# Kernel tuning notes

Measured on AMD Instinct MI355X. Metric: run time of the kernel, lower is better.

Reference implementation:

```python
import jax, jax.numpy as jnp
import numpy as np

B, D, K, NCLS, BANK = 1024, 256, 8, 71, 32


def setup_inputs() -> dict:
    key = jax.random.key(0)
    ks = jax.random.split(key, 8)
    p = lambda k: jax.random.normal(k, (D, D), jnp.float32) * 0.02  # trunc_normal std=0.02 approx
    z = jnp.zeros((D,), jnp.float32)
    return {
        "target_token": jax.random.normal(ks[0], (B, D), jnp.float32),
        "fea_bank": jax.random.normal(ks[1], (NCLS, BANK, D), jnp.float32),
        "W_e1": p(ks[2]), "b_e1": z,
        "W_o1": p(ks[3]), "b_o1": z,
        "W_e2": p(ks[4]), "b_e2": z,
        "W_o2": p(ks[5]), "b_o2": z,
        "W_f1": p(ks[6]),
        "W_f2": p(ks[7]),
    }


def reference(target_token, fea_bank, W_e1, b_e1, W_o1, b_o1,
              W_e2, b_e2, W_o2, b_o2, W_f1, W_f2):
    lin = lambda x, W, b: x @ W.T + b  # torch nn.Linear convention

    # class-mean bank and euclidean cdist [B, NCLS]
    fea_mean = fea_bank.mean(axis=1)                              # [C, D]
    d2 = (jnp.sum(target_token ** 2, -1, keepdims=True)
          - 2.0 * target_token @ fea_mean.T
          + jnp.sum(fea_mean ** 2, -1))
    dist = jnp.sqrt(jnp.maximum(d2, 0.0))
    _, idx = jax.lax.top_k(-dist, K)                              # k smallest -> [B, K]

    # stage 1: blend with nearest class means
    nearest_means = fea_mean[idx]                                 # [B, K, D]
    e1 = jax.nn.gelu(lin(nearest_means - target_token[:, None], W_e1, b_e1),
                     approximate=False)
    w1 = e1 @ W_f1.T
    e1 = e1 * jax.nn.softmax(w1, axis=1)                          # softmax over K
    off1 = jnp.tanh(lin(target_token[:, None] + e1, W_o1, b_o1))
    s1 = (1.0 + off1) * target_token[:, None]                     # [B, K, D]

    # stage 2: blend with full intra-class banks of selected classes
    feats = fea_bank[idx]                                         # [B, K, BANK, D]
    e2 = jax.nn.gelu(lin(feats - s1[:, :, None], W_e2, b_e2), approximate=False)
    w2 = e2 @ W_f2.T
    e2 = e2 * jax.nn.softmax(w2, axis=2)                          # softmax over BANK
    off2 = jnp.tanh(lin(s1[:, :, None] + e2, W_o2, b_o2))
    s2 = ((1.0 + off2) * s1[:, :, None]).sum(axis=2)              # [B, K, D]

    return (s1, s2)
```

## Files before the change

### kernel.cpp

```cpp
#include <hip/hip_runtime.h>
#include <hip/hip_bf16.h>

#define BB 1024
#define DD 256
#define KK 8
#define NCLS_ 71
#define BANK_ 32
#define BKROWS (BB*KK)
#define NBROWS (NCLS_*BANK_)

typedef __bf16 bf16x8 __attribute__((ext_vector_type(8)));
typedef __bf16 bf16x4 __attribute__((ext_vector_type(4)));
typedef float f32x4 __attribute__((ext_vector_type(4)));

__device__ __forceinline__ float gelu_fast(float x) {
    float z = __expf(-1.702f * x);
    return x * __builtin_amdgcn_rcpf(1.0f + z);
}
__device__ __forceinline__ float tanh_fast(float y) {
    float z = __expf(2.0f * y);
    return 1.0f - 2.0f * __builtin_amdgcn_rcpf(z + 1.0f);
}
__device__ __forceinline__ int swz(int row, int colByte) {
    return (row * 512 + colByte) ^ ((row & 7) << 4);
}

template<int MT, int NT>
__device__ __forceinline__ void gemm_tile(const __bf16* __restrict__ Wg,
                                          const char* Ab, int m_base, int n_base,
                                          int lane, f32x4 (&acc)[MT][NT])
{
    #pragma unroll
    for (int ks = 0; ks < 8; ++ks) {
        bf16x8 a[MT];
        #pragma unroll
        for (int mt = 0; mt < MT; ++mt) {
            int row = m_base + mt*16 + (lane & 15);
            int cb  = ks*64 + ((lane >> 4) << 4);
            a[mt] = *reinterpret_cast<const bf16x8*>(Ab + swz(row, cb));
        }
        #pragma unroll
        for (int nt = 0; nt < NT; ++nt) {
            int n  = n_base + nt*16 + (lane & 15);
            int k0 = ks*32 + ((lane >> 4) << 3);
            bf16x8 b = *reinterpret_cast<const bf16x8*>(Wg + n*DD + k0);
            #pragma unroll
            for (int mt = 0; mt < MT; ++mt)
                acc[mt][nt] = __builtin_amdgcn_mfma_f32_16x16x32_bf16(a[mt], b, acc[mt][nt], 0, 0, 0);
        }
    }
}

__global__ __launch_bounds__(256) void k_prep(
    const float* __restrict__ We1f, const float* __restrict__ Wo1f,
    const float* __restrict__ We2f, const float* __restrict__ Wo2f,
    const float* __restrict__ Wf1f, const float* __restrict__ Wf2f,
    const float* __restrict__ fb,
    __bf16* __restrict__ We1, __bf16* __restrict__ Wo1,
    __bf16* __restrict__ We2, __bf16* __restrict__ Wo2,
    __bf16* __restrict__ Wf1, __bf16* __restrict__ Wf2,
    __bf16* __restrict__ fbb, float* __restrict__ fmean)
{
    int b = blockIdx.x, tid = threadIdx.x;
    if (b < 384) {
        int w = b >> 6;
        const float* s; __bf16* d;
        switch (w) {
            case 0: s = We1f; d = We1; break;
            case 1: s = Wo1f; d = Wo1; break;
            case 2: s = We2f; d = We2; break;
            case 3: s = Wo2f; d = Wo2; break;
            case 4: s = Wf1f; d = Wf1; break;
            default: s = Wf2f; d = Wf2; break;
        }
        int i = (b & 63)*256 + tid;
        float4 v = reinterpret_cast<const float4*>(s)[i];
        bf16x4 o = {(__bf16)v.x, (__bf16)v.y, (__bf16)v.z, (__bf16)v.w};
        *reinterpret_cast<bf16x4*>(d + i*4) = o;
    } else if (b < 952) {
        int i = (b - 384)*256 + tid;
        float4 v = reinterpret_cast<const float4*>(fb)[i];
        bf16x4 o = {(__bf16)v.x, (__bf16)v.y, (__bf16)v.z, (__bf16)v.w};
        *reinterpret_cast<bf16x4*>(fbb + i*4) = o;
    } else {
        int c = b - 952, d = tid;
        float s = 0.f;
        #pragma unroll
        for (int j = 0; j < BANK_; ++j) s += fb[(c*BANK_ + j)*DD + d];
        fmean[c*DD + d] = s * (1.0f / BANK_);
    }
}

__global__ __launch_bounds__(128) void k_stage1(
    const float* __restrict__ tgt, const float* __restrict__ fmean,
    int* __restrict__ idxg,
    const __bf16* __restrict__ We1, const float* __restrict__ be1,
    const __bf16* __restrict__ Wf1,
    const __bf16* __restrict__ Wo1, const float* __restrict__ bo1,
    float* __restrict__ out_s1, __bf16* __restrict__ s1b)
{
    __shared__ __bf16 As[16*256];
    __shared__ float tl[256];
    __shared__ float d2s[NCLS_ + 1];
    __shared__ int cls[8];
    char* Ab = (char*)As;
    int tid = threadIdx.x, lane = tid & 63, wid = tid >> 6;
    int b = blockIdx.x;
    if (tid < 64) reinterpret_cast<float4*>(tl)[tid] = reinterpret_cast<const float4*>(tgt + b*DD)[tid];
    {
        uint4 zz = {0u,0u,0u,0u};
        #pragma unroll
        for (int i = 0; i < 2; ++i) {
            int f = i*128 + tid;
            int row = 8 + (f >> 5), c = f & 31;
            *reinterpret_cast<uint4*>(Ab + swz(row, c*16)) = zz;
        }
    }
    __syncthreads();
    {
        float t0 = tl[lane], t1 = tl[64+lane], t2 = tl[128+lane], t3 = tl[192+lane];
        int cbeg = wid*36, cend = cbeg + 36 - wid;
        for (int c = cbeg; c < cend; ++c) {
            const float* m = fmean + c*DD;
            float a0 = t0 - m[lane], a1 = t1 - m[64+lane];
            float a2 = t2 - m[128+lane], a3 = t3 - m[192+lane];
            float p = a0*a0 + a1*a1 + a2*a2 + a3*a3;
            #pragma unroll
            for (int o = 32; o > 0; o >>= 1) p += __shfl_xor(p, o);
            if (lane == 0) d2s[c] = p;
        }
    }
    __syncthreads();
    if (tid == 0) {
        #pragma unroll
        for (int t = 0; t < KK; ++t) {
            float best = 3.4e38f; int bi = 0;
            for (int c = 0; c < NCLS_; ++c) { float v = d2s[c]; if (v < best) { best = v; bi = c; } }
            d2s[bi] = 3.4e38f;
            cls[t] = bi;
            idxg[b*KK + t] = bi;
        }
    }
    __syncthreads();
    int c16 = tid & 31, q = tid >> 5;
    #pragma unroll
    for (int i = 0; i < 2; ++i) {
        int row = i*4 + q;
        const float* mb = fmean + cls[row]*DD + c16*8;
        const float* tb = tl + c16*8;
        float4 m0 = *(const float4*)mb, m1 = *(const float4*)(mb+4);
        float4 t0 = *(const float4*)tb, t1 = *(const float4*)(tb+4);
        bf16x8 o = {(__bf16)(m0.x-t0.x), (__bf16)(m0.y-t0.y), (__bf16)(m0.z-t0.z), (__bf16)(m0.w-t0.w),
                    (__bf16)(m1.x-t1.x), (__bf16)(m1.y-t1.y), (__bf16)(m1.z-t1.z), (__bf16)(m1.w-t1.w)};
        *reinterpret_cast<bf16x8*>(Ab + swz(row, c16*16)) = o;
    }
    __syncthreads();
    int n_base = wid * 128;
    int qr = lane >> 4;
    const f32x4 z = {0.f, 0.f, 0.f, 0.f};
    f32x4 acc[1][8];
    #pragma unroll
    for (int nt = 0; nt < 8; ++nt) acc[0][nt] = z;
    gemm_tile<1,8>(We1, Ab, 0, n_base, lane, acc);
    float e1reg[8][4];
    #pragma unroll
    for (int nt = 0; nt < 8; ++nt)
        #pragma unroll
        for (int r = 0; r < 4; ++r) {
            int col = n_base + nt*16 + (lane & 15);
            e1reg[nt][r] = gelu_fast(acc[0][nt][r] + be1[col]);
        }
    __syncthreads();
    if (qr < 2)
        #pragma unroll
        for (int nt = 0; nt < 8; ++nt)
            #pragma unroll
            for (int r = 0; r < 4; ++r) {
                int row = qr*4 + r;
                int col = n_base + nt*16 + (lane & 15);
                *(__bf16*)(Ab + swz(row, col*2)) = (__bf16)e1reg[nt][r];
            }
    __syncthreads();
    f32x4 acc2[1][8];
    #pragma unroll
    for (int nt = 0; nt < 8; ++nt) acc2[0][nt] = z;
    gemm_tile<1,8>(Wf1, Ab, 0, n_base, lane, acc2);
    float a2v[8][4];
    #pragma unroll
    for (int nt = 0; nt < 8; ++nt) {
        float mx = fmaxf(fmaxf(acc2[0][nt][0], acc2[0][nt][1]),
                         fmaxf(acc2[0][nt][2], acc2[0][nt][3]));
        mx = fmaxf(mx, __shfl_xor(mx, 16));
        float p[4], s = 0.f;
        #pragma unroll
        for (int r = 0; r < 4; ++r) { p[r] = __expf(acc2[0][nt][r] - mx); s += p[r]; }
        s += __shfl_xor(s, 16);
        float inv = __builtin_amdgcn_rcpf(s);
        int col = n_base + nt*16 + (lane & 15);
        #pragma unroll
        for (int r = 0; r < 4; ++r)
            a2v[nt][r] = tl[col] + e1reg[nt][r] * p[r] * inv;
    }
    __syncthreads();
    if (qr < 2)
        #pragma unroll
        for (int nt = 0; nt < 8; ++nt)
            #pragma unroll
            for (int r = 0; r < 4; ++r) {
                int row = qr*4 + r;
                int col = n_base + nt*16 + (lane & 15);
                *(__bf16*)(Ab + swz(row, col*2)) = (__bf16)a2v[nt][r];
            }
    __syncthreads();
    #pragma unroll
    for (int nt = 0; nt < 8; ++nt) acc[0][nt] = z;
    gemm_tile<1,8>(Wo1, Ab, 0, n_base, lane, acc);
    if (qr < 2)
        #pragma unroll
        for (int nt = 0; nt < 8; ++nt)
            #pragma unroll
            for (int r = 0; r < 4; ++r) {
                int row = qr*4 + r;
                int col = n_base + nt*16 + (lane & 15);
                float off = tanh_fast(acc[0][nt][r] + bo1[col]);
                float s1v = (1.0f + off) * tl[col];
                int g = (b*8 + row)*DD + col;
                out_s1[g] = s1v;
                s1b[g] = (__bf16)s1v;
            }
}

__global__ __launch_bounds__(256) void k_gemms(
    const __bf16* __restrict__ fbb, const __bf16* __restrict__ s1b,
    const __bf16* __restrict__ We2, const __bf16* __restrict__ Wo2,
    const float* __restrict__ be2, const float* __restrict__ bo2,
    __bf16* __restrict__ FBe2b, __bf16* __restrict__ S1We2, __bf16* __restrict__ S1Wo2)
{
    __shared__ __bf16 As[32*256];
    char* Ab = (char*)As;
    int tid = threadIdx.x, lane = tid & 63, wid = tid >> 6;
    bool fbpath = blockIdx.x < 71;
    const __bf16* A = fbpath ? fbb : s1b;
    int m0 = fbpath ? blockIdx.x * 32 : (blockIdx.x - 71) * 32;
    #pragma unroll
    for (int i = 0; i < 4; ++i) {
        int f = i*256 + tid;
        int row = f >> 5, c16 = f & 31;
        uint4 v = *reinterpret_cast<const uint4*>(A + (size_t)(m0+row)*DD + c16*8);
        *reinterpret_cast<uint4*>(Ab + swz(row, c16*16)) = v;
    }
    __syncthreads();
    int n_base = wid * 64;
    const f32x4 z = {0.f, 0.f, 0.f, 0.f};
    f32x4 acc[2][4];
    #pragma unroll
    for (int mt = 0; mt < 2; ++mt)
        #pragma unroll
        for (int nt = 0; nt < 4; ++nt) acc[mt][nt] = z;
    gemm_tile<2,4>(We2, Ab, 0, n_base, lane, acc);
    #pragma unroll
    for (int mt = 0; mt < 2; ++mt)
        #pragma unroll
        for (int nt = 0; nt < 4; ++nt)
            #pragma unroll
            for (int r = 0; r < 4; ++r) {
                int row = mt*16 + ((lane >> 4) << 2) + r;
                int col = n_base + nt*16 + (lane & 15);
                if (fbpath) FBe2b[(size_t)(m0+row)*DD + col] = (__bf16)(acc[mt][nt][r] + be2[col]);
                else        S1We2[(size_t)(m0+row)*DD + col] = (__bf16)acc[mt][nt][r];
            }
    if (!fbpath) {
        #pragma unroll
        for (int mt = 0; mt < 2; ++mt)
            #pragma unroll
            for (int nt = 0; nt < 4; ++nt) acc[mt][nt] = z;
        gemm_tile<2,4>(Wo2, Ab, 0, n_base, lane, acc);
        #pragma unroll
        for (int mt = 0; mt < 2; ++mt)
            #pragma unroll
            for (int nt = 0; nt < 4; ++nt)
                #pragma unroll
                for (int r = 0; r < 4; ++r) {
                    int row = mt*16 + ((lane >> 4) << 2) + r;
                    int col = n_base + nt*16 + (lane & 15);
                    S1Wo2[(size_t)(m0+row)*DD + col] = (__bf16)(acc[mt][nt][r] + bo2[col]);
                }
    }
}

__global__ __launch_bounds__(512, 4) void k_stage2(
    const int* __restrict__ idx,
    const __bf16* __restrict__ FBe2b,
    const __bf16* __restrict__ S1We2,
    const __bf16* __restrict__ S1Wo2,
    const __bf16* __restrict__ Wf2,
    const __bf16* __restrict__ Wo2,
    const float* __restrict__ s1,
    float* __restrict__ s2)
{
    __shared__ __bf16 As[64*256];
    char* Ab = (char*)As;
    int tid = threadIdx.x, lane = tid & 63, wid = tid >> 6;
    int u0 = blockIdx.x * 2;
    int cls0 = idx[u0], cls1 = idx[u0+1];
    int c16 = tid & 31, q = tid >> 5;
    #pragma unroll
    for (int i = 0; i < 4; ++i) {
        int row = i*16 + q;
        int unit = row >> 5, j = row & 31;
        int cls = unit ? cls1 : cls0;
        bf16x8 f = *reinterpret_cast<const bf16x8*>(FBe2b + ((size_t)cls*BANK_ + j)*DD + c16*8);
        bf16x8 g = *reinterpret_cast<const bf16x8*>(S1We2 + (size_t)(u0+unit)*DD + c16*8);
        bf16x8 o;
        #pragma unroll
        for (int e = 0; e < 8; ++e) o[e] = (__bf16)gelu_fast((float)f[e] - (float)g[e]);
        *reinterpret_cast<bf16x8*>(Ab + swz(row, c16*16)) = o;
    }
    __syncthreads();
    int n_base = wid * 32;
    const f32x4 z = {0.f, 0.f, 0.f, 0.f};
    f32x4 acc[4][2];
    #pragma unroll
    for (int mt = 0; mt < 4; ++mt)
        #pragma unroll
        for (int nt = 0; nt < 2; ++nt) acc[mt][nt] = z;
    gemm_tile<4,2>(Wf2, Ab, 0, n_base, lane, acc);
    float inv_[2][2];
    #pragma unroll
    for (int unit = 0; unit < 2; ++unit)
        #pragma unroll
        for (int nt = 0; nt < 2; ++nt) {
            float mx = -3.4e38f;
            #pragma unroll
            for (int mh = 0; mh < 2; ++mh)
                #pragma unroll
                for (int r = 0; r < 4; ++r) mx = fmaxf(mx, acc[unit*2+mh][nt][r]);
            mx = fmaxf(mx, __shfl_xor(mx, 16));
            mx = fmaxf(mx, __shfl_xor(mx, 32));
            float s = 0.f;
            #pragma unroll
            for (int mh = 0; mh < 2; ++mh)
                #pragma unroll
                for (int r = 0; r < 4; ++r) {
                    float e = __expf(acc[unit*2+mh][nt][r] - mx);
                    acc[unit*2+mh][nt][r] = e;
                    s += e;
                }
            s += __shfl_xor(s, 16);
            s += __shfl_xor(s, 32);
            inv_[unit][nt] = __builtin_amdgcn_rcpf(s);
        }
    __syncthreads();
    #pragma unroll
    for (int mt = 0; mt < 4; ++mt)
        #pragma unroll
        for (int nt = 0; nt < 2; ++nt)
            #pragma unroll
            for (int r = 0; r < 4; ++r) {
                int row = mt*16 + ((lane >> 4) << 2) + r;
                int col = n_base + nt*16 + (lane & 15);
                __bf16* p16 = (__bf16*)(Ab + swz(row, col*2));
                *p16 = (__bf16)((float)*p16 * acc[mt][nt][r] * inv_[mt>>1][nt]);
            }
    __syncthreads();
    #pragma unroll
    for (int mt = 0; mt < 4; ++mt)
        #pragma unroll
        for (int nt = 0; nt < 2; ++nt) acc[mt][nt] = z;
    gemm_tile<4,2>(Wo2, Ab, 0, n_base, lane, acc);
    #pragma unroll
    for (int unit = 0; unit < 2; ++unit) {
        size_t u = u0 + unit;
        #pragma unroll
        for (int nt = 0; nt < 2; ++nt) {
            int col = n_base + nt*16 + (lane & 15);
            float srow = (float)S1Wo2[u*DD + col];
            float cs = 0.f;
            #pragma unroll
            for (int mh = 0; mh < 2; ++mh)
                #pragma unroll
                for (int r = 0; r < 4; ++r) cs += tanh_fast(acc[unit*2+mh][nt][r] + srow);
            cs += __shfl_xor(cs, 16);
            cs += __shfl_xor(cs, 32);
            if ((lane >> 4) == 0)
                s2[u*DD + col] = s1[u*DD + col] * (32.0f + cs);
        }
    }
}

extern "C" void kernel_launch(void* const* d_in, const int* in_sizes, int n_in,
                              void* d_out, int out_size, void* d_ws, size_t ws_size,
                              hipStream_t stream)
{
    const float* tgt  = (const float*)d_in[0];
    const float* fb   = (const float*)d_in[1];
    const float* We1f = (const float*)d_in[2];
    const float* be1  = (const float*)d_in[3];
    const float* Wo1f = (const float*)d_in[4];
    const float* bo1  = (const float*)d_in[5];
    const float* We2f = (const float*)d_in[6];
    const float* be2  = (const float*)d_in[7];
    const float* Wo2f = (const float*)d_in[8];
    const float* bo2  = (const float*)d_in[9];
    const float* Wf1f = (const float*)d_in[10];
    const float* Wf2f = (const float*)d_in[11];

    char* ws = (char*)d_ws;
    size_t off = 0;
    auto alloc = [&](size_t bytes) { char* p = ws + off; off += (bytes + 255) & ~255ull; return p; };
    float*  fmean = (float*)alloc(NCLS_*DD*4);
    int*    idx   = (int*)alloc(BB*KK*4);
    __bf16* We1   = (__bf16*)alloc(DD*DD*2);
    __bf16* Wo1   = (__bf16*)alloc(DD*DD*2);
    __bf16* We2   = (__bf16*)alloc(DD*DD*2);
    __bf16* Wo2   = (__bf16*)alloc(DD*DD*2);
    __bf16* Wf1   = (__bf16*)alloc(DD*DD*2);
    __bf16* Wf2   = (__bf16*)alloc(DD*DD*2);
    __bf16* fbb   = (__bf16*)alloc((size_t)NBROWS*DD*2);
    __bf16* s1b   = (__bf16*)alloc((size_t)BKROWS*DD*2);
    __bf16* FBe2b = (__bf16*)alloc((size_t)NBROWS*DD*2);
    __bf16* S1We2 = (__bf16*)alloc((size_t)BKROWS*DD*2);
    __bf16* S1Wo2 = (__bf16*)alloc((size_t)BKROWS*DD*2);

    float* out_s1 = (float*)d_out;
    float* out_s2 = out_s1 + (size_t)BKROWS*DD;

    k_prep<<<1023, 256, 0, stream>>>(We1f, Wo1f, We2f, Wo2f, Wf1f, Wf2f, fb,
                                     We1, Wo1, We2, Wo2, Wf1, Wf2, fbb, fmean);
    k_stage1<<<BB, 128, 0, stream>>>(tgt, fmean, idx, We1, be1, Wf1, Wo1, bo1, out_s1, s1b);
    k_gemms<<<71 + BKROWS/32, 256, 0, stream>>>(fbb, s1b, We2, Wo2, be2, bo2,
                                                FBe2b, S1We2, S1Wo2);
    k_stage2<<<BKROWS/2, 512, 0, stream>>>(idx, FBe2b, S1We2, S1Wo2, Wf2, Wo2, out_s1, out_s2);
}
```

Measured before the change: 260.7 us.

## Parallelize top-k with wavefront shuffles and double stage-2 block size

```diff
diff --git a/kernel.cpp b/kernel.cpp
--- a/kernel.cpp
+++ b/kernel.cpp
@@ -131,14 +131,22 @@
         }
     }
     __syncthreads();
-    if (tid == 0) {
+    if (wid == 0) {
+        float d0 = d2s[lane];
+        float d1 = (lane < NCLS_ - 64) ? d2s[64 + lane] : 3.4e38f;
         #pragma unroll
         for (int t = 0; t < KK; ++t) {
-            float best = 3.4e38f; int bi = 0;
-            for (int c = 0; c < NCLS_; ++c) { float v = d2s[c]; if (v < best) { best = v; bi = c; } }
-            d2s[bi] = 3.4e38f;
-            cls[t] = bi;
-            idxg[b*KK + t] = bi;
+            float bd; int bi;
+            if (d0 <= d1) { bd = d0; bi = lane; } else { bd = d1; bi = 64 + lane; }
+            #pragma unroll
+            for (int o = 1; o < 64; o <<= 1) {
+                float od = __shfl_xor(bd, o);
+                int   oi = __shfl_xor(bi, o);
+                if (od < bd || (od == bd && oi < bi)) { bd = od; bi = oi; }
+            }
+            if (lane == 0) { cls[t] = bi; idxg[b*KK + t] = bi; }
+            if (bi == lane)      d0 = 3.4e38f;
+            if (bi == 64 + lane) d1 = 3.4e38f;
         }
     }
     __syncthreads();
@@ -288,7 +296,7 @@
     }
 }
 
-__global__ __launch_bounds__(512, 4) void k_stage2(
+__global__ __launch_bounds__(1024, 8) void k_stage2(
     const int* __restrict__ idx,
     const __bf16* __restrict__ FBe2b,
     const __bf16* __restrict__ S1We2,
@@ -298,18 +306,19 @@
     const float* __restrict__ s1,
     float* __restrict__ s2)
 {
-    __shared__ __bf16 As[64*256];
+    __shared__ __bf16 As[128*256];
+    __shared__ int clss[4];
     char* Ab = (char*)As;
     int tid = threadIdx.x, lane = tid & 63, wid = tid >> 6;
-    int u0 = blockIdx.x * 2;
-    int cls0 = idx[u0], cls1 = idx[u0+1];
+    int u0 = blockIdx.x * 4;
+    if (tid < 4) clss[tid] = idx[u0 + tid];
+    __syncthreads();
     int c16 = tid & 31, q = tid >> 5;
     #pragma unroll
     for (int i = 0; i < 4; ++i) {
-        int row = i*16 + q;
+        int row = i*32 + q;
         int unit = row >> 5, j = row & 31;
-        int cls = unit ? cls1 : cls0;
-        bf16x8 f = *reinterpret_cast<const bf16x8*>(FBe2b + ((size_t)cls*BANK_ + j)*DD + c16*8);
+        bf16x8 f = *reinterpret_cast<const bf16x8*>(FBe2b + ((size_t)clss[unit]*BANK_ + j)*DD + c16*8);
         bf16x8 g = *reinterpret_cast<const bf16x8*>(S1We2 + (size_t)(u0+unit)*DD + c16*8);
         bf16x8 o;
         #pragma unroll
@@ -317,24 +326,26 @@
         *reinterpret_cast<bf16x8*>(Ab + swz(row, c16*16)) = o;
     }
     __syncthreads();
-    int n_base = wid * 32;
+    int h = wid >> 3;
+    int m_base = h * 64;
+    int n_base = (wid & 7) * 32;
     const f32x4 z = {0.f, 0.f, 0.f, 0.f};
     f32x4 acc[4][2];
     #pragma unroll
     for (int mt = 0; mt < 4; ++mt)
         #pragma unroll
         for (int nt = 0; nt < 2; ++nt) acc[mt][nt] = z;
-    gemm_tile<4,2>(Wf2, Ab, 0, n_base, lane, acc);
+    gemm_tile<4,2>(Wf2, Ab, m_base, n_base, lane, acc);
     float inv_[2][2];
     #pragma unroll
-    for (int unit = 0; unit < 2; ++unit)
+    for (int uiw = 0; uiw < 2; ++uiw)
         #pragma unroll
         for (int nt = 0; nt < 2; ++nt) {
             float mx = -3.4e38f;
             #pragma unroll
             for (int mh = 0; mh < 2; ++mh)
                 #pragma unroll
-                for (int r = 0; r < 4; ++r) mx = fmaxf(mx, acc[unit*2+mh][nt][r]);
+                for (int r = 0; r < 4; ++r) mx = fmaxf(mx, acc[uiw*2+mh][nt][r]);
             mx = fmaxf(mx, __shfl_xor(mx, 16));
             mx = fmaxf(mx, __shfl_xor(mx, 32));
             float s = 0.f;
@@ -342,13 +353,13 @@
             for (int mh = 0; mh < 2; ++mh)
                 #pragma unroll
                 for (int r = 0; r < 4; ++r) {
-                    float e = __expf(acc[unit*2+mh][nt][r] - mx);
-                    acc[unit*2+mh][nt][r] = e;
+                    float e = __expf(acc[uiw*2+mh][nt][r] - mx);
+                    acc[uiw*2+mh][nt][r] = e;
                     s += e;
                 }
             s += __shfl_xor(s, 16);
             s += __shfl_xor(s, 32);
-            inv_[unit][nt] = __builtin_amdgcn_rcpf(s);
+            inv_[uiw][nt] = __builtin_amdgcn_rcpf(s);
         }
     __syncthreads();
     #pragma unroll
@@ -357,7 +368,7 @@
         for (int nt = 0; nt < 2; ++nt)
             #pragma unroll
             for (int r = 0; r < 4; ++r) {
-                int row = mt*16 + ((lane >> 4) << 2) + r;
+                int row = m_base + mt*16 + ((lane >> 4) << 2) + r;
                 int col = n_base + nt*16 + (lane & 15);
                 __bf16* p16 = (__bf16*)(Ab + swz(row, col*2));
                 *p16 = (__bf16)((float)*p16 * acc[mt][nt][r] * inv_[mt>>1][nt]);
@@ -367,10 +378,10 @@
     for (int mt = 0; mt < 4; ++mt)
         #pragma unroll
         for (int nt = 0; nt < 2; ++nt) acc[mt][nt] = z;
-    gemm_tile<4,2>(Wo2, Ab, 0, n_base, lane, acc);
-    #pragma unroll
-    for (int unit = 0; unit < 2; ++unit) {
-        size_t u = u0 + unit;
+    gemm_tile<4,2>(Wo2, Ab, m_base, n_base, lane, acc);
+    #pragma unroll
+    for (int uiw = 0; uiw < 2; ++uiw) {
+        size_t u = u0 + 2*h + uiw;
         #pragma unroll
         for (int nt = 0; nt < 2; ++nt) {
             int col = n_base + nt*16 + (lane & 15);
@@ -379,7 +390,7 @@
             #pragma unroll
             for (int mh = 0; mh < 2; ++mh)
                 #pragma unroll
-                for (int r = 0; r < 4; ++r) cs += tanh_fast(acc[unit*2+mh][nt][r] + srow);
+                for (int r = 0; r < 4; ++r) cs += tanh_fast(acc[uiw*2+mh][nt][r] + srow);
             cs += __shfl_xor(cs, 16);
             cs += __shfl_xor(cs, 32);
             if ((lane >> 4) == 0)
@@ -430,5 +441,5 @@
     k_stage1<<<BB, 128, 0, stream>>>(tgt, fmean, idx, We1, be1, Wf1, Wo1, bo1, out_s1, s1b);
     k_gemms<<<71 + BKROWS/32, 256, 0, stream>>>(fbb, s1b, We2, Wo2, be2, bo2,
                                                 FBe2b, S1We2, S1Wo2);
-    k_stage2<<<BKROWS/2, 512, 0, stream>>>(idx, FBe2b, S1We2, S1Wo2, Wf2, Wo2, out_s1, out_s2);
-}
+    k_stage2<<<BKROWS/4, 1024, 0, stream>>>(idx, FBe2b, S1We2, S1Wo2, Wf2, Wo2, out_s1, out_s2);
+}
```

Result: slower. 364.0 us (+39.6%).

## Fuse stage-2 projection GEMMs into stage1 kernel and parallelize top-k selection

Applied to the files above, without the earlier changes.

```diff
diff --git a/kernel.cpp b/kernel.cpp
--- a/kernel.cpp
+++ b/kernel.cpp
@@ -97,7 +97,11 @@
     const __bf16* __restrict__ We1, const float* __restrict__ be1,
     const __bf16* __restrict__ Wf1,
     const __bf16* __restrict__ Wo1, const float* __restrict__ bo1,
-    float* __restrict__ out_s1, __bf16* __restrict__ s1b)
+    const __bf16* __restrict__ We2, const float* __restrict__ be2,
+    const __bf16* __restrict__ Wo2, const float* __restrict__ bo2,
+    const __bf16* __restrict__ fbb,
+    float* __restrict__ out_s1,
+    __bf16* __restrict__ FBe2b, __bf16* __restrict__ S1We2, __bf16* __restrict__ S1Wo2)
 {
     __shared__ __bf16 As[16*256];
     __shared__ float tl[256];
@@ -105,6 +109,34 @@
     __shared__ int cls[8];
     char* Ab = (char*)As;
     int tid = threadIdx.x, lane = tid & 63, wid = tid >> 6;
+    const f32x4 z = {0.f, 0.f, 0.f, 0.f};
+
+    if (blockIdx.x >= BB) {
+        int m0 = (blockIdx.x - BB) * 16;
+        int c16 = tid & 31;
+        #pragma unroll
+        for (int i = 0; i < 4; ++i) {
+            int row = i*4 + (tid >> 5);
+            uint4 v = *reinterpret_cast<const uint4*>(fbb + (size_t)(m0+row)*DD + c16*8);
+            *reinterpret_cast<uint4*>(Ab + swz(row, c16*16)) = v;
+        }
+        __syncthreads();
+        int n_base = wid * 128;
+        f32x4 acc[1][8];
+        #pragma unroll
+        for (int nt = 0; nt < 8; ++nt) acc[0][nt] = z;
+        gemm_tile<1,8>(We2, Ab, 0, n_base, lane, acc);
+        #pragma unroll
+        for (int nt = 0; nt < 8; ++nt)
+            #pragma unroll
+            for (int r = 0; r < 4; ++r) {
+                int row = ((lane >> 4) << 2) + r;
+                int col = n_base + nt*16 + (lane & 15);
+                FBe2b[(size_t)(m0+row)*DD + col] = (__bf16)(acc[0][nt][r] + be2[col]);
+            }
+        return;
+    }
+
     int b = blockIdx.x;
     if (tid < 64) reinterpret_cast<float4*>(tl)[tid] = reinterpret_cast<const float4*>(tgt + b*DD)[tid];
     {
@@ -131,14 +163,22 @@
         }
     }
     __syncthreads();
-    if (tid == 0) {
+    if (wid == 0) {
+        float d0 = d2s[lane];
+        float d1 = (lane < NCLS_ - 64) ? d2s[64 + lane] : 3.4e38f;
         #pragma unroll
         for (int t = 0; t < KK; ++t) {
-            float best = 3.4e38f; int bi = 0;
-            for (int c = 0; c < NCLS_; ++c) { float v = d2s[c]; if (v < best) { best = v; bi = c; } }
-            d2s[bi] = 3.4e38f;
-            cls[t] = bi;
-            idxg[b*KK + t] = bi;
+            float bd; int bi;
+            if (d0 <= d1) { bd = d0; bi = lane; } else { bd = d1; bi = 64 + lane; }
+            #pragma unroll
+            for (int o = 1; o < 64; o <<= 1) {
+                float od = __shfl_xor(bd, o);
+                int   oi = __shfl_xor(bi, o);
+                if (od < bd || (od == bd && oi < bi)) { bd = od; bi = oi; }
+            }
+            if (lane == 0) { cls[t] = bi; idxg[b*KK + t] = bi; }
+            if (bi == lane)      d0 = 3.4e38f;
+            if (bi == 64 + lane) d1 = 3.4e38f;
         }
     }
     __syncthreads();
@@ -157,7 +197,6 @@
     __syncthreads();
     int n_base = wid * 128;
     int qr = lane >> 4;
-    const f32x4 z = {0.f, 0.f, 0.f, 0.f};
     f32x4 acc[1][8];
     #pragma unroll
     for (int nt = 0; nt < 8; ++nt) acc[0][nt] = z;
@@ -215,6 +254,7 @@
     #pragma unroll
     for (int nt = 0; nt < 8; ++nt) acc[0][nt] = z;
     gemm_tile<1,8>(Wo1, Ab, 0, n_base, lane, acc);
+    float s1vr[8][4];
     if (qr < 2)
         #pragma unroll
         for (int nt = 0; nt < 8; ++nt)
@@ -224,68 +264,44 @@
                 int col = n_base + nt*16 + (lane & 15);
                 float off = tanh_fast(acc[0][nt][r] + bo1[col]);
                 float s1v = (1.0f + off) * tl[col];
-                int g = (b*8 + row)*DD + col;
-                out_s1[g] = s1v;
-                s1b[g] = (__bf16)s1v;
-            }
-}
-
-__global__ __launch_bounds__(256) void k_gemms(
-    const __bf16* __restrict__ fbb, const __bf16* __restrict__ s1b,
-    const __bf16* __restrict__ We2, const __bf16* __restrict__ Wo2,
-    const float* __restrict__ be2, const float* __restrict__ bo2,
-    __bf16* __restrict__ FBe2b, __bf16* __restrict__ S1We2, __bf16* __restrict__ S1Wo2)
-{
-    __shared__ __bf16 As[32*256];
-    char* Ab = (char*)As;
-    int tid = threadIdx.x, lane = tid & 63, wid = tid >> 6;
-    bool fbpath = blockIdx.x < 71;
-    const __bf16* A = fbpath ? fbb : s1b;
-    int m0 = fbpath ? blockIdx.x * 32 : (blockIdx.x - 71) * 32;
-    #pragma unroll
-    for (int i = 0; i < 4; ++i) {
-        int f = i*256 + tid;
-        int row = f >> 5, c16 = f & 31;
-        uint4 v = *reinterpret_cast<const uint4*>(A + (size_t)(m0+row)*DD + c16*8);
-        *reinterpret_cast<uint4*>(Ab + swz(row, c16*16)) = v;
-    }
-    __syncthreads();
-    int n_base = wid * 64;
-    const f32x4 z = {0.f, 0.f, 0.f, 0.f};
-    f32x4 acc[2][4];
-    #pragma unroll
-    for (int mt = 0; mt < 2; ++mt)
-        #pragma unroll
-        for (int nt = 0; nt < 4; ++nt) acc[mt][nt] = z;
-    gemm_tile<2,4>(We2, Ab, 0, n_base, lane, acc);
-    #pragma unroll
-    for (int mt = 0; mt < 2; ++mt)
-        #pragma unroll
-        for (int nt = 0; nt < 4; ++nt)
-            #pragma unroll
-            for (int r = 0; r < 4; ++r) {
-                int row = mt*16 + ((lane >> 4) << 2) + r;
-                int col = n_base + nt*16 + (lane & 15);
-                if (fbpath) FBe2b[(size_t)(m0+row)*DD + col] = (__bf16)(acc[mt][nt][r] + be2[col]);
-                else        S1We2[(size_t)(m0+row)*DD + col] = (__bf16)acc[mt][nt][r];
-            }
-    if (!fbpath) {
-        #pragma unroll
-        for (int mt = 0; mt < 2; ++mt)
-            #pragma unroll
-            for (int nt = 0; nt < 4; ++nt) acc[mt][nt] = z;
-        gemm_tile<2,4>(Wo2, Ab, 0, n_base, lane, acc);
-        #pragma unroll
-        for (int mt = 0; mt < 2; ++mt)
-            #pragma unroll
-            for (int nt = 0; nt < 4; ++nt)
-                #pragma unroll
-                for (int r = 0; r < 4; ++r) {
-                    int row = mt*16 + ((lane >> 4) << 2) + r;
-                    int col = n_base + nt*16 + (lane & 15);
-                    S1Wo2[(size_t)(m0+row)*DD + col] = (__bf16)(acc[mt][nt][r] + bo2[col]);
-                }
-    }
+                out_s1[(b*8 + row)*DD + col] = s1v;
+                s1vr[nt][r] = s1v;
+            }
+    __syncthreads();
+    if (qr < 2)
+        #pragma unroll
+        for (int nt = 0; nt < 8; ++nt)
+            #pragma unroll
+            for (int r = 0; r < 4; ++r) {
+                int row = qr*4 + r;
+                int col = n_base + nt*16 + (lane & 15);
+                *(__bf16*)(Ab + swz(row, col*2)) = (__bf16)s1vr[nt][r];
+            }
+    __syncthreads();
+    #pragma unroll
+    for (int nt = 0; nt < 8; ++nt) acc[0][nt] = z;
+    gemm_tile<1,8>(We2, Ab, 0, n_base, lane, acc);
+    if (qr < 2)
+        #pragma unroll
+        for (int nt = 0; nt < 8; ++nt)
+            #pragma unroll
+            for (int r = 0; r < 4; ++r) {
+                int row = qr*4 + r;
+                int col = n_base + nt*16 + (lane & 15);
+                S1We2[(size_t)(b*8 + row)*DD + col] = (__bf16)acc[0][nt][r];
+            }
+    #pragma unroll
+    for (int nt = 0; nt < 8; ++nt) acc2[0][nt] = z;
+    gemm_tile<1,8>(Wo2, Ab, 0, n_base, lane, acc2);
+    if (qr < 2)
+        #pragma unroll
+        for (int nt = 0; nt < 8; ++nt)
+            #pragma unroll
+            for (int r = 0; r < 4; ++r) {
+                int row = qr*4 + r;
+                int col = n_base + nt*16 + (lane & 15);
+                S1Wo2[(size_t)(b*8 + row)*DD + col] = (__bf16)(acc2[0][nt][r] + bo2[col]);
+            }
 }
 
 __global__ __launch_bounds__(512, 4) void k_stage2(
@@ -303,6 +319,16 @@
     int tid = threadIdx.x, lane = tid & 63, wid = tid >> 6;
     int u0 = blockIdx.x * 2;
     int cls0 = idx[u0], cls1 = idx[u0+1];
+    int n_base = wid * 32;
+    float srowp[2][2], s1p[2][2];
+    #pragma unroll
+    for (int uu = 0; uu < 2; ++uu)
+        #pragma unroll
+        for (int nt = 0; nt < 2; ++nt) {
+            int col = n_base + nt*16 + (lane & 15);
+            srowp[uu][nt] = (float)S1Wo2[(size_t)(u0+uu)*DD + col];
+            s1p[uu][nt]  = s1[(size_t)(u0+uu)*DD + col];
+        }
     int c16 = tid & 31, q = tid >> 5;
     #pragma unroll
     for (int i = 0; i < 4; ++i) {
@@ -317,7 +343,6 @@
         *reinterpret_cast<bf16x8*>(Ab + swz(row, c16*16)) = o;
     }
     __syncthreads();
-    int n_base = wid * 32;
     const f32x4 z = {0.f, 0.f, 0.f, 0.f};
     f32x4 acc[4][2];
     #pragma unroll
@@ -327,14 +352,14 @@
     gemm_tile<4,2>(Wf2, Ab, 0, n_base, lane, acc);
     float inv_[2][2];
     #pragma unroll
-    for (int unit = 0; unit < 2; ++unit)
+    for (int uw = 0; uw < 2; ++uw)
         #pragma unroll
         for (int nt = 0; nt < 2; ++nt) {
             float mx = -3.4e38f;
             #pragma unroll
             for (int mh = 0; mh < 2; ++mh)
                 #pragma unroll
-                for (int r = 0; r < 4; ++r) mx = fmaxf(mx, acc[unit*2+mh][nt][r]);
+                for (int r = 0; r < 4; ++r) mx = fmaxf(mx, acc[uw*2+mh][nt][r]);
             mx = fmaxf(mx, __shfl_xor(mx, 16));
             mx = fmaxf(mx, __shfl_xor(mx, 32));
             float s = 0.f;
@@ -342,13 +367,13 @@
             for (int mh = 0; mh < 2; ++mh)
                 #pragma unroll
                 for (int r = 0; r < 4; ++r) {
-                    float e = __expf(acc[unit*2+mh][nt][r] - mx);
-                    acc[unit*2+mh][nt][r] = e;
+                    float e = __expf(acc[uw*2+mh][nt][r] - mx);
+                    acc[uw*2+mh][nt][r] = e;
                     s += e;
                 }
             s += __shfl_xor(s, 16);
             s += __shfl_xor(s, 32);
-            inv_[unit][nt] = __builtin_amdgcn_rcpf(s);
+            inv_[uw][nt] = __builtin_amdgcn_rcpf(s);
         }
     __syncthreads();
     #pragma unroll
@@ -369,21 +394,21 @@
         for (int nt = 0; nt < 2; ++nt) acc[mt][nt] = z;
     gemm_tile<4,2>(Wo2, Ab, 0, n_base, lane, acc);
     #pragma unroll
-    for (int unit = 0; unit < 2; ++unit) {
-        size_t u = u0 + unit;
+    for (int uw = 0; uw < 2; ++uw) {
+        size_t u = u0 + uw;
         #pragma unroll
         for (int nt = 0; nt < 2; ++nt) {
             int col = n_base + nt*16 + (lane & 15);
-            float srow = (float)S1Wo2[u*DD + col];
+            float srow = srowp[uw][nt];
             float cs = 0.f;
             #pragma unroll
             for (int mh = 0; mh < 2; ++mh)
                 #pragma unroll
-                for (int r = 0; r < 4; ++r) cs += tanh_fast(acc[unit*2+mh][nt][r] + srow);
+                for (int r = 0; r < 4; ++r) cs += tanh_fast(acc[uw*2+mh][nt][r] + srow);
             cs += __shfl_xor(cs, 16);
             cs += __shfl_xor(cs, 32);
             if ((lane >> 4) == 0)
-                s2[u*DD + col] = s1[u*DD + col] * (32.0f + cs);
+                s2[u*DD + col] = s1p[uw][nt] * (32.0f + cs);
         }
     }
 }
@@ -417,7 +442,6 @@
     __bf16* Wf1   = (__bf16*)alloc(DD*DD*2);
     __bf16* Wf2   = (__bf16*)alloc(DD*DD*2);
     __bf16* fbb   = (__bf16*)alloc((size_t)NBROWS*DD*2);
-    __bf16* s1b   = (__bf16*)alloc((size_t)BKROWS*DD*2);
     __bf16* FBe2b = (__bf16*)alloc((size_t)NBROWS*DD*2);
     __bf16* S1We2 = (__bf16*)alloc((size_t)BKROWS*DD*2);
     __bf16* S1Wo2 = (__bf16*)alloc((size_t)BKROWS*DD*2);
@@ -427,8 +451,9 @@
 
     k_prep<<<1023, 256, 0, stream>>>(We1f, Wo1f, We2f, Wo2f, Wf1f, Wf2f, fb,
                                      We1, Wo1, We2, Wo2, Wf1, Wf2, fbb, fmean);
-    k_stage1<<<BB, 128, 0, stream>>>(tgt, fmean, idx, We1, be1, Wf1, Wo1, bo1, out_s1, s1b);
-    k_gemms<<<71 + BKROWS/32, 256, 0, stream>>>(fbb, s1b, We2, Wo2, be2, bo2,
-                                                FBe2b, S1We2, S1Wo2);
+    k_stage1<<<BB + NBROWS/16, 128, 0, stream>>>(tgt, fmean, idx,
+                                                 We1, be1, Wf1, Wo1, bo1,
+                                                 We2, be2, Wo2, bo2, fbb,
+                                                 out_s1, FBe2b, S1We2, S1Wo2);
     k_stage2<<<BKROWS/2, 512, 0, stream>>>(idx, FBe2b, S1We2, S1Wo2, Wf2, Wo2, out_s1, out_s2);
 }
```

New measurement: 264.4 us. Within noise of the previous version (+1.4%).
